# Kernel tuning notes

Hardware: AMD Instinct MI355X
Metric: run time of the kernel (lower is better)

The kernel has to match this reference:

```python
import jax, jax.numpy as jnp
import numpy as np

B, H, W, C = 32, 256, 256, 3
FLAT = (H // 4) * (W // 4) * 64  # 64*64*64 = 262144 after two stride-2 SAME convs


def _conv(x, k, b, stride):
    y = jax.lax.conv_general_dilated(
        x, k, (stride, stride), 'SAME',
        dimension_numbers=('NHWC', 'HWIO', 'NHWC'))
    return jax.nn.relu(y + b)


def _grid_sample(img, theta):
    # STN: build normalized affine grid from theta [B,2,3], bilinear sample with
    # zero padding for out-of-bounds (GridSampler2D semantics).
    b, h, w, c = img.shape
    xs = (2.0 * jnp.arange(w, dtype=img.dtype) + 1.0) / w - 1.0
    ys = (2.0 * jnp.arange(h, dtype=img.dtype) + 1.0) / h - 1.0
    X, Y = jnp.meshgrid(xs, ys)                      # [H,W]
    base = jnp.stack([X, Y, jnp.ones_like(X)], -1)   # [H,W,3]
    g = jnp.einsum('bij,hwj->bhwi', theta, base)     # [B,H,W,2] (x,y) in [-1,1]
    px = (g[..., 0] + 1.0) * 0.5 * w - 0.5
    py = (g[..., 1] + 1.0) * 0.5 * h - 0.5
    x0 = jnp.floor(px); y0 = jnp.floor(py)
    wx1 = px - x0; wx0 = 1.0 - wx1
    wy1 = py - y0; wy0 = 1.0 - wy1

    bidx = jnp.arange(b)[:, None, None]

    def gather(yi, xi):
        valid = (xi >= 0) & (xi < w) & (yi >= 0) & (yi < h)
        xc = jnp.clip(xi, 0, w - 1).astype(jnp.int32)
        yc = jnp.clip(yi, 0, h - 1).astype(jnp.int32)
        v = img[bidx, yc, xc]                        # [B,H,W,C]
        return v * valid[..., None].astype(img.dtype)

    out = (gather(y0, x0) * (wy0 * wx0)[..., None]
           + gather(y0, x0 + 1) * (wy0 * wx1)[..., None]
           + gather(y0 + 1, x0) * (wy1 * wx0)[..., None]
           + gather(y0 + 1, x0 + 1) * (wy1 * wx1)[..., None])
    return out


def setup_inputs() -> dict:
    key = jax.random.key(0)
    ks = jax.random.split(key, 9)
    s = 0.05
    return {
        'inputs': jax.random.uniform(ks[0], (B, H, W, C), jnp.float32),
        'k1': jax.random.normal(ks[1], (3, 3, C, 32), jnp.float32) * s,
        'b1': jnp.zeros((32,), jnp.float32),
        'k2': jax.random.normal(ks[2], (3, 3, 32, 64), jnp.float32) * s,
        'b2': jnp.zeros((64,), jnp.float32),
        'w1': jax.random.normal(ks[3], (FLAT, 128), jnp.float32) * 0.002,
        'd1': jnp.zeros((128,), jnp.float32),
        'w2': jax.random.normal(ks[4], (128, 6), jnp.float32) * s,
        'd2': jnp.asarray([1, 0, 0, 0, 1, 0], jnp.float32),  # identity-ish bias
    }


def reference(inputs, k1, b1, k2, b2, w1, d1, w2, d2):
    x = _conv(inputs, k1, b1, 2)          # [B,H/2,W/2,32]
    x = _conv(x, k2, b2, 2)               # [B,H/4,W/4,64]
    x = x.reshape(x.shape[0], -1)         # [B,FLAT]
    x = jax.nn.relu(x @ w1 + d1)          # [B,128]
    theta = (x @ w2 + d2).reshape(-1, 2, 3)
    return _grid_sample(inputs, theta)
```

## Files before the change

kernel.cpp:

```cpp
#include <hip/hip_runtime.h>

#define IN_H 256
#define IN_W 256
#define C0   3
#define C1   32
#define H1   128
#define C2   64
#define H2   64
#define NB   32
#define K_FLAT (H2*H2*C2)
#define NHID 128

#define A1_IDX(b,p,y,ci,x2) ((((((size_t)(b)*2 + (p))*H1 + (y))*C1 + (ci))*64) + (x2))

__global__ __launch_bounds__(256)
void conv1_k(const float* __restrict__ in, const float* __restrict__ k1,
             const float* __restrict__ b1, float* __restrict__ a1p) {
  const int tid = threadIdx.x;
  const int ox  = tid & 127;
  const int cg  = __builtin_amdgcn_readfirstlane((tid >> 7) * 16);
  const int oy  = blockIdx.x;
  const int b   = blockIdx.y;

  float acc[16];
#pragma unroll
  for (int co = 0; co < 16; ++co) acc[co] = b1[cg + co];

#pragma unroll
  for (int dy = 0; dy < 3; ++dy) {
    const int iy  = 2*oy + dy;
    if (iy >= IN_H) continue;
#pragma unroll
    for (int dx = 0; dx < 3; ++dx) {
      const int ix  = 2*ox + dx;
      const bool ok = ix < IN_W;
      const int ixc = ok ? ix : (IN_W-1);
      const float* ip = in + ((size_t)(b*IN_H + iy)*IN_W + ixc)*C0;
      const float m  = ok ? 1.f : 0.f;
      const float v0 = ip[0] * m;
      const float v1 = ip[1] * m;
      const float v2 = ip[2] * m;
      const float* wp = k1 + (size_t)((dy*3+dx)*C0)*C1 + cg;
#pragma unroll
      for (int co = 0; co < 16; ++co)
        acc[co] = fmaf(v0, wp[co],
                  fmaf(v1, wp[C1+co],
                  fmaf(v2, wp[2*C1+co], acc[co])));
    }
  }
  const int p  = ox & 1;
  const int x2 = ox >> 1;
#pragma unroll
  for (int co = 0; co < 16; ++co)
    a1p[A1_IDX(b, p, oy, cg + co, x2)] = fmaxf(acc[co], 0.f);
}

#define CONV2_DY_LOOP(EDGE_)                                                   \
  _Pragma("unroll")                                                            \
  for (int dy = 0; dy < 3; ++dy) {                                             \
    int iy = 2*oy + dy;                                                        \
    float rm = 1.f;                                                            \
    if (EDGE_) { if (iy >= H1) { iy = H1 - 1; rm = 0.f; } }                    \
    const float* r0 = a1p + A1_IDX(b, 0, iy, 0, 0) + 2*lx;                     \
    const float* r1 = a1p + A1_IDX(b, 1, iy, 0, 0) + 2*lx;                     \
    const float* wp = k2 + (size_t)(dy*3*C1)*C2 + cg16;                        \
    const float m2 = EDGE_ ? rm * xm : xm;                                     \
    _Pragma("unroll 4")                                                        \
    for (int ci = 0; ci < C1; ++ci) {                                          \
      const float2 Av = *(const float2*)(r0 + (size_t)ci*64);                  \
      const float  A2 = r0[(size_t)ci*64 + 2];                                 \
      const float2 Bv = *(const float2*)(r1 + (size_t)ci*64);                  \
      const float ax = EDGE_ ? Av.x*rm : Av.x;                                 \
      const float ay = EDGE_ ? Av.y*rm : Av.y;                                 \
      const float bx = EDGE_ ? Bv.x*rm : Bv.x;                                 \
      const float by = EDGE_ ? Bv.y*rm : Bv.y;                                 \
      const float a2v = A2 * m2;                                               \
      const float* w0  = wp + (size_t)ci*C2;                                   \
      const float* w1r = wp + (size_t)(C1 + ci)*C2;                            \
      const float* w2r = wp + (size_t)(2*C1 + ci)*C2;                          \
      _Pragma("unroll")                                                        \
      for (int co = 0; co < 16; ++co) {                                        \
        acc0[co] = fmaf(ax, w0[co],                                            \
                   fmaf(bx, w1r[co],                                           \
                   fmaf(ay,  w2r[co], acc0[co])));                             \
        acc1[co] = fmaf(ay, w0[co],                                            \
                   fmaf(by, w1r[co],                                           \
                   fmaf(a2v, w2r[co], acc1[co])));                             \
      }                                                                        \
    }                                                                          \
  }

__global__ __launch_bounds__(256)
void conv2_k(const float* __restrict__ a1p, const float* __restrict__ k2,
             const float* __restrict__ b2, float* __restrict__ a2) {
  const int tid  = threadIdx.x;
  const int lane = tid & 63;
  const int lx   = lane & 31;
  const int oys  = lane >> 5;
  const int cg16 = __builtin_amdgcn_readfirstlane((tid >> 6) * 16);
  const int oy   = blockIdx.x * 2 + oys;
  const int b    = blockIdx.y;

  float acc0[16], acc1[16];
#pragma unroll
  for (int co = 0; co < 16; ++co) { acc0[co] = b2[cg16 + co]; acc1[co] = acc0[co]; }

  const float xm = (lx == 31) ? 0.f : 1.f;

  if (blockIdx.x == 31) {
    CONV2_DY_LOOP(1)
  } else {
    CONV2_DY_LOOP(0)
  }

  float* op = a2 + ((size_t)((b*H2 + oy)*H2) + 2*lx)*C2 + cg16;
#pragma unroll
  for (int g = 0; g < 4; ++g) {
    float4 o0;
    o0.x = fmaxf(acc0[4*g+0], 0.f);
    o0.y = fmaxf(acc0[4*g+1], 0.f);
    o0.z = fmaxf(acc0[4*g+2], 0.f);
    o0.w = fmaxf(acc0[4*g+3], 0.f);
    ((float4*)op)[g] = o0;
    float4 o1;
    o1.x = fmaxf(acc1[4*g+0], 0.f);
    o1.y = fmaxf(acc1[4*g+1], 0.f);
    o1.z = fmaxf(acc1[4*g+2], 0.f);
    o1.w = fmaxf(acc1[4*g+3], 0.f);
    ((float4*)(op + C2))[g] = o1;
  }
}

#define FC1_G   2048
#define KSPAN   (K_FLAT / FC1_G)
#define GC1     16

__global__ __launch_bounds__(256)
void fc1_partial_k(const float* __restrict__ a2, const float* __restrict__ w1,
                   float* __restrict__ partial) {
  __shared__ __align__(16) float xT[KSPAN*36];
  const int tid = threadIdx.x;
  const int q   = tid & 31;
  const int bo  = tid >> 5;
  const int k0  = blockIdx.x * KSPAN;

  {
    const int lb  = tid >> 3;
    const int lkq = tid & 7;
#pragma unroll
    for (int j = 0; j < 4; ++j) {
      const int k4 = lkq*4 + j*32;
      float4 t = *(const float4*)(a2 + (size_t)lb*K_FLAT + k0 + k4);
      xT[(k4+0)*36 + lb] = t.x;
      xT[(k4+1)*36 + lb] = t.y;
      xT[(k4+2)*36 + lb] = t.z;
      xT[(k4+3)*36 + lb] = t.w;
    }
  }
  __syncthreads();

  float4 a0 = make_float4(0.f,0.f,0.f,0.f), a1v = a0, a2v = a0, a3v = a0;
#pragma unroll 8
  for (int k = 0; k < KSPAN; ++k) {
    const float4 w4 = *(const float4*)(w1 + (size_t)(k0 + k)*NHID + 4*q);
    const float4 xb = *(const float4*)&xT[k*36 + 4*bo];
    a0.x = fmaf(xb.x, w4.x, a0.x); a0.y = fmaf(xb.x, w4.y, a0.y);
    a0.z = fmaf(xb.x, w4.z, a0.z); a0.w = fmaf(xb.x, w4.w, a0.w);
    a1v.x = fmaf(xb.y, w4.x, a1v.x); a1v.y = fmaf(xb.y, w4.y, a1v.y);
    a1v.z = fmaf(xb.y, w4.z, a1v.z); a1v.w = fmaf(xb.y, w4.w, a1v.w);
    a2v.x = fmaf(xb.z, w4.x, a2v.x); a2v.y = fmaf(xb.z, w4.y, a2v.y);
    a2v.z = fmaf(xb.z, w4.z, a2v.z); a2v.w = fmaf(xb.z, w4.w, a2v.w);
    a3v.x = fmaf(xb.w, w4.x, a3v.x); a3v.y = fmaf(xb.w, w4.y, a3v.y);
    a3v.z = fmaf(xb.w, w4.z, a3v.z); a3v.w = fmaf(xb.w, w4.w, a3v.w);
  }

  float* pp = partial + (size_t)blockIdx.x*(NB*NHID) + 4*q;
  *(float4*)(pp + (4*bo+0)*NHID) = a0;
  *(float4*)(pp + (4*bo+1)*NHID) = a1v;
  *(float4*)(pp + (4*bo+2)*NHID) = a2v;
  *(float4*)(pp + (4*bo+3)*NHID) = a3v;
}

__global__ __launch_bounds__(128)
void fc1_reduce1_k(const float* __restrict__ partial, float* __restrict__ partial2) {
  const int t  = blockIdx.x*128 + threadIdx.x;
  const int gc = blockIdx.y;
  float s = 0.f;
#pragma unroll 8
  for (int g = gc*(FC1_G/GC1); g < gc*(FC1_G/GC1) + (FC1_G/GC1); ++g)
    s += partial[(size_t)g*(NB*NHID) + t];
  partial2[(size_t)gc*(NB*NHID) + t] = s;
}

__global__ __launch_bounds__(256)
void fc1_reduce2_k(const float* __restrict__ partial2, const float* __restrict__ d1,
                   float* __restrict__ h) {
  const int t = blockIdx.x*256 + threadIdx.x;
  float s = 0.f;
#pragma unroll
  for (int gc = 0; gc < GC1; ++gc) s += partial2[(size_t)gc*(NB*NHID) + t];
  h[t] = fmaxf(s + d1[t & (NHID-1)], 0.f);
}

__global__ __launch_bounds__(192)
void theta_k(const float* __restrict__ h, const float* __restrict__ w2,
             const float* __restrict__ d2, float* __restrict__ theta) {
  const int t = threadIdx.x;
  if (t >= NB*6) return;
  const int b = t / 6, j = t % 6;
  float s0 = 0.f, s1 = 0.f, s2 = 0.f, s3 = 0.f;
  for (int n = 0; n < NHID; n += 4) {
    s0 = fmaf(h[b*NHID + n+0], w2[(n+0)*6 + j], s0);
    s1 = fmaf(h[b*NHID + n+1], w2[(n+1)*6 + j], s1);
    s2 = fmaf(h[b*NHID + n+2], w2[(n+2)*6 + j], s2);
    s3 = fmaf(h[b*NHID + n+3], w2[(n+3)*6 + j], s3);
  }
  theta[t] = (s0 + s1) + (s2 + s3) + d2[j];
}

__global__ __launch_bounds__(256)
void sample_k(const float* __restrict__ img, const float* __restrict__ theta,
              float* __restrict__ out) {
  const int x = threadIdx.x;
  const int y = blockIdx.x & (IN_H-1);
  const int b = blockIdx.x >> 8;
  const float* tp = theta + b*6;
  const float t0 = tp[0], t1 = tp[1], t2 = tp[2];
  const float t3 = tp[3], t4 = tp[4], t5 = tp[5];

  const float xs = (2.f*x + 1.f)*(1.f/IN_W) - 1.f;
  const float ys = (2.f*y + 1.f)*(1.f/IN_H) - 1.f;
  const float gx = fmaf(t0, xs, fmaf(t1, ys, t2));
  const float gy = fmaf(t3, xs, fmaf(t4, ys, t5));
  const float px = fmaf(gx + 1.f, 0.5f*IN_W, -0.5f);
  const float py = fmaf(gy + 1.f, 0.5f*IN_H, -0.5f);

  const float x0f = floorf(px), y0f = floorf(py);
  const int ix0 = (int)x0f, iy0 = (int)y0f;
  const float wx1 = px - x0f, wx0 = 1.f - wx1;
  const float wy1 = py - y0f, wy0 = 1.f - wy1;

  float r = 0.f, g = 0.f, bl = 0.f;
  const float* ib = img + (size_t)b*IN_H*IN_W*C0;

  auto tap = [&](int yi, int xi, float w) {
    const bool v = (xi >= 0) && (xi < IN_W) && (yi >= 0) && (yi < IN_H);
    const int xc = xi < 0 ? 0 : (xi > IN_W-1 ? IN_W-1 : xi);
    const int yc = yi < 0 ? 0 : (yi > IN_H-1 ? IN_H-1 : yi);
    const float* p = ib + ((size_t)yc*IN_W + xc)*C0;
    if (v) {
      r  = fmaf(w, p[0], r);
      g  = fmaf(w, p[1], g);
      bl = fmaf(w, p[2], bl);
    }
  };
  tap(iy0,   ix0,   wy0*wx0);
  tap(iy0,   ix0+1, wy0*wx1);
  tap(iy0+1, ix0,   wy1*wx0);
  tap(iy0+1, ix0+1, wy1*wx1);

  float* op = out + ((size_t)(b*IN_H + y)*IN_W + x)*C0;
  op[0] = r; op[1] = g; op[2] = bl;
}

extern "C" void kernel_launch(void* const* d_in, const int* in_sizes, int n_in,
                              void* d_out, int out_size, void* d_ws, size_t ws_size,
                              hipStream_t stream) {
  const float* in = (const float*)d_in[0];
  const float* k1 = (const float*)d_in[1];
  const float* b1 = (const float*)d_in[2];
  const float* k2 = (const float*)d_in[3];
  const float* b2 = (const float*)d_in[4];
  const float* w1 = (const float*)d_in[5];
  const float* d1 = (const float*)d_in[6];
  const float* w2 = (const float*)d_in[7];
  const float* d2 = (const float*)d_in[8];
  float* out = (float*)d_out;
  float* ws  = (float*)d_ws;

  float* a1p     = ws;
  float* a2      = ws + (size_t)16777216;
  float* partial = ws;
  float* part2   = ws + (size_t)8388608;
  float* h       = ws + (size_t)8454144;
  float* th      = ws + (size_t)8458240;

  hipLaunchKernelGGL(conv1_k,       dim3(128, 32), dim3(256), 0, stream, in, k1, b1, a1p);
  hipLaunchKernelGGL(conv2_k,       dim3(32, 32),  dim3(256), 0, stream, a1p, k2, b2, a2);
  hipLaunchKernelGGL(fc1_partial_k, dim3(FC1_G),   dim3(256), 0, stream, a2, w1, partial);
  hipLaunchKernelGGL(fc1_reduce1_k, dim3(32, GC1), dim3(128), 0, stream, partial, part2);
  hipLaunchKernelGGL(fc1_reduce2_k, dim3(16),      dim3(256), 0, stream, part2, d1, h);
  hipLaunchKernelGGL(theta_k,       dim3(1),       dim3(192), 0, stream, h, w2, d2, th);
  hipLaunchKernelGGL(sample_k,      dim3(NB*IN_H), dim3(256), 0, stream, in, th, out);
}
```

Measured before the change: 366.5 us.

## Stage conv2 weight slice in LDS and remap blocks to channel groups

The conv2 kernel now gives each block a single 16-channel output group and 8 output rows, one pair of rows per wave. The block first copies that group's 3x3x32x16 weight slice into shared memory in a packed [dy][ci][dx][co] layout. The inner loop then reads weights from LDS instead of scalar global loads, and the ci unroll drops from 4 to 2. The goal is cheaper, contiguous weight access, at the cost of a staging pass, a barrier, and waves in a block no longer sharing the same activation rows.

```diff
diff --git a/kernel.cpp b/kernel.cpp
--- a/kernel.cpp
+++ b/kernel.cpp
@@ -63,9 +63,9 @@
     if (EDGE_) { if (iy >= H1) { iy = H1 - 1; rm = 0.f; } }                    \
     const float* r0 = a1p + A1_IDX(b, 0, iy, 0, 0) + 2*lx;                     \
     const float* r1 = a1p + A1_IDX(b, 1, iy, 0, 0) + 2*lx;                     \
-    const float* wp = k2 + (size_t)(dy*3*C1)*C2 + cg16;                        \
+    const float* wdy = wl + dy*(C1*3*16);                                      \
     const float m2 = EDGE_ ? rm * xm : xm;                                     \
-    _Pragma("unroll 4")                                                        \
+    _Pragma("unroll 2")                                                        \
     for (int ci = 0; ci < C1; ++ci) {                                          \
       const float2 Av = *(const float2*)(r0 + (size_t)ci*64);                  \
       const float  A2 = r0[(size_t)ci*64 + 2];                                 \
@@ -75,9 +75,9 @@
       const float bx = EDGE_ ? Bv.x*rm : Bv.x;                                 \
       const float by = EDGE_ ? Bv.y*rm : Bv.y;                                 \
       const float a2v = A2 * m2;                                               \
-      const float* w0  = wp + (size_t)ci*C2;                                   \
-      const float* w1r = wp + (size_t)(C1 + ci)*C2;                            \
-      const float* w2r = wp + (size_t)(2*C1 + ci)*C2;                          \
+      const float* w0  = wdy + ci*48;                                          \
+      const float* w1r = w0 + 16;                                              \
+      const float* w2r = w0 + 32;                                              \
       _Pragma("unroll")                                                        \
       for (int co = 0; co < 16; ++co) {                                        \
         acc0[co] = fmaf(ax, w0[co],                                            \
@@ -93,27 +93,42 @@
 __global__ __launch_bounds__(256)
 void conv2_k(const float* __restrict__ a1p, const float* __restrict__ k2,
              const float* __restrict__ b2, float* __restrict__ a2) {
+  __shared__ __align__(16) float wl[3*C1*3*16];
   const int tid  = threadIdx.x;
+  const int cg   = blockIdx.x >> 3;
+  const int q    = blockIdx.x & 7;
+  const int b    = blockIdx.y;
+
+  for (int i = tid; i < 3*C1*3*16; i += 256) {
+    const int coo = i & 15;
+    const int t   = i >> 4;
+    const int dx  = t % 3;
+    const int u   = t / 3;
+    const int ci  = u & 31;
+    const int dy  = u >> 5;
+    wl[i] = k2[((size_t)((dy*3+dx)*C1 + ci))*C2 + 16*cg + coo];
+  }
+  __syncthreads();
+
+  const int w    = tid >> 6;
   const int lane = tid & 63;
   const int lx   = lane & 31;
   const int oys  = lane >> 5;
-  const int cg16 = __builtin_amdgcn_readfirstlane((tid >> 6) * 16);
-  const int oy   = blockIdx.x * 2 + oys;
-  const int b    = blockIdx.y;
+  const int oy   = q*8 + w*2 + oys;
 
   float acc0[16], acc1[16];
 #pragma unroll
-  for (int co = 0; co < 16; ++co) { acc0[co] = b2[cg16 + co]; acc1[co] = acc0[co]; }
+  for (int co = 0; co < 16; ++co) { acc0[co] = b2[16*cg + co]; acc1[co] = acc0[co]; }
 
   const float xm = (lx == 31) ? 0.f : 1.f;
 
-  if (blockIdx.x == 31) {
+  if (q == 7) {
     CONV2_DY_LOOP(1)
   } else {
     CONV2_DY_LOOP(0)
   }
 
-  float* op = a2 + ((size_t)((b*H2 + oy)*H2) + 2*lx)*C2 + cg16;
+  float* op = a2 + ((size_t)((b*H2 + oy)*H2) + 2*lx)*C2 + 16*cg;
 #pragma unroll
   for (int g = 0; g < 4; ++g) {
     float4 o0;
```

Measured after the change: 393.0 us. 7.2% more time.
